# Kernel optimization log

Hardware: AMD Instinct MI355X
Metric: run time of the kernel (lower is better)

Reference implementation:

```python
import jax, jax.numpy as jnp
import numpy as np

EMBED_DIM = 1024
HEAD_DIM = 64
B, S = 8, 2048


def setup_inputs() -> dict:
    key = jax.random.key(0)
    ks = jax.random.split(key, 8)
    s_in = 1.0 / np.sqrt(EMBED_DIM)
    return {
        "x": jax.random.normal(ks[0], (B, S, EMBED_DIM), dtype=jnp.float32),
        "y": jax.random.normal(ks[1], (B, S, EMBED_DIM), dtype=jnp.float32),
        "Wq": jax.random.normal(ks[2], (EMBED_DIM, HEAD_DIM), dtype=jnp.float32) * s_in,
        "bq": jnp.zeros((HEAD_DIM,), dtype=jnp.float32),
        "Wk": jax.random.normal(ks[3], (EMBED_DIM, HEAD_DIM), dtype=jnp.float32) * s_in,
        "bk": jnp.zeros((HEAD_DIM,), dtype=jnp.float32),
        "Wv": jax.random.normal(ks[4], (EMBED_DIM, HEAD_DIM), dtype=jnp.float32) * s_in,
        "bv": jnp.zeros((HEAD_DIM,), dtype=jnp.float32),
    }


def reference(x, y, Wq, bq, Wk, bk, Wv, bv):
    # single-head attention; mask=True -> tril applied PRE-softmax (zeros, not -inf)
    q = jnp.einsum("bse,eh->bsh", y, Wq) + bq  # [B,S,H]
    k = jnp.einsum("bse,eh->bsh", x, Wk) + bk
    v = jnp.einsum("bse,eh->bsh", x, Wv) + bv
    scale = 1.0 / jnp.sqrt(jnp.float32(HEAD_DIM))
    scores = jnp.einsum("bqh,bkh->bqk", q, k) * scale  # [B,S,S]
    scores = jnp.tril(scores)  # faithful: zero upper triangle BEFORE softmax
    attn = jax.nn.softmax(scores, axis=-1)
    return jnp.einsum("bqk,bkh->bqh", attn, v)  # [B,S,H]
```

## Files before the change

### kernel.cpp

```cpp
#include <hip/hip_runtime.h>

#define SEQ 2048
#define EMB 1024
#define HD 64

typedef _Float16 f16x8 __attribute__((ext_vector_type(8)));
typedef _Float16 f16x4 __attribute__((ext_vector_type(4)));
typedef float f32x4 __attribute__((ext_vector_type(4)));

__device__ __forceinline__ f32x4 mfma32(f16x8 a, f16x8 b, f32x4 c) {
    return __builtin_amdgcn_mfma_f32_16x16x32_f16(a, b, c, 0, 0, 0);
}
__device__ __forceinline__ f32x4 mfma16(f16x4 a, f16x4 b, f32x4 c) {
    return __builtin_amdgcn_mfma_f32_16x16x16f16(a, b, c, 0, 0, 0);
}

__global__ __launch_bounds__(256) void wcvt_kernel(
    const float* __restrict__ Wq, const float* __restrict__ Wk,
    const float* __restrict__ Wv, _Float16* __restrict__ Wf)
{
    const int m = blockIdx.x >> 2, nt = blockIdx.x & 3, kq = blockIdx.y;
    const float* __restrict__ W = (m == 0) ? Wq : (m == 1) ? Wk : Wv;
    const int tid = threadIdx.x;
    #pragma unroll
    for (int i = 0; i < 2; ++i) {
        int linear = i * 256 + tid;
        int kc = kq * 8 + (linear >> 6), ln = linear & 63;
        int q8 = (ln >> 4) * 8, l = ln & 15;
        f16x8 w;
        #pragma unroll
        for (int j = 0; j < 8; ++j)
            w[j] = (_Float16)W[(size_t)(kc * 32 + q8 + j) * 64 + nt * 16 + l];
        *(f16x8*)&Wf[((size_t)((m * 4 + nt) * 32 + kc)) * 512 + (size_t)ln * 8] = w;
    }
}

__global__ __launch_bounds__(512, 2) void proj_kernel(
    const float* __restrict__ x, const float* __restrict__ y,
    const _Float16* __restrict__ Wf,
    const float* __restrict__ bq, const float* __restrict__ bk,
    const float* __restrict__ bv,
    _Float16* __restrict__ Qb, _Float16* __restrict__ Kf,
    _Float16* __restrict__ Vf, float* __restrict__ Vts)
{
    const int mode = blockIdx.y;
    const int r0 = blockIdx.x * 128;
    const int tid = threadIdx.x;
    const int wave = tid >> 6, lane = tid & 63;
    const int l15 = lane & 15, quad = lane >> 4;

    __shared__ float TL[128][65];

    const float* __restrict__ src = mode ? x : y;
    const _Float16* __restrict__ WA = Wf + (mode ? 65536 : 0);
    const _Float16* __restrict__ WB = Wf + 131072;

    f32x4 zero = {0.f, 0.f, 0.f, 0.f};
    f32x4 acc0[4], acc1[4];
    #pragma unroll
    for (int i = 0; i < 4; ++i) { acc0[i] = zero; acc1[i] = zero; }

    const float* arow = src + (size_t)(r0 + wave * 16 + l15) * 1024 + quad * 8;
    const int lo8 = lane * 8;

    float4 Aa0, Aa1, Ab0, Ab1;
    f16x8 BqA[4], BqB[4], BvA[4], BvB[4];

    auto LDA = [&](float4& x0, float4& x1, int ch) {
        const float4* p = (const float4*)(arow + ch * 32);
        x0 = p[0]; x1 = p[1];
    };
    auto LDBq = [&](f16x8* d, int ch) {
        #pragma unroll
        for (int nt = 0; nt < 4; ++nt)
            d[nt] = *(const f16x8*)&WA[((size_t)(nt * 32 + ch)) * 512 + lo8];
    };
    auto LDBv = [&](f16x8* d, int ch) {
        #pragma unroll
        for (int nt = 0; nt < 4; ++nt)
            d[nt] = *(const f16x8*)&WB[((size_t)(nt * 32 + ch)) * 512 + lo8];
    };
    auto CVT = [&](float4 a0, float4 a1) {
        f16x8 af;
        af[0] = (_Float16)a0.x; af[1] = (_Float16)a0.y;
        af[2] = (_Float16)a0.z; af[3] = (_Float16)a0.w;
        af[4] = (_Float16)a1.x; af[5] = (_Float16)a1.y;
        af[6] = (_Float16)a1.z; af[7] = (_Float16)a1.w;
        return af;
    };

    LDA(Aa0, Aa1, 0); LDBq(BqA, 0); if (mode) LDBv(BvA, 0);
    LDA(Ab0, Ab1, 1); LDBq(BqB, 1); if (mode) LDBv(BvB, 1);

    #pragma unroll 1
    for (int ch = 0; ch < 32; ch += 2) {
        {
            f16x8 af = CVT(Aa0, Aa1);
            #pragma unroll
            for (int nt = 0; nt < 4; ++nt)
                acc0[nt] = mfma32(af, BqA[nt], acc0[nt]);
            if (mode) {
                #pragma unroll
                for (int nt = 0; nt < 4; ++nt)
                    acc1[nt] = mfma32(af, BvA[nt], acc1[nt]);
            }
            const int nx = (ch + 2) & 31;
            LDA(Aa0, Aa1, nx); LDBq(BqA, nx); if (mode) LDBv(BvA, nx);
        }
        {
            f16x8 af = CVT(Ab0, Ab1);
            #pragma unroll
            for (int nt = 0; nt < 4; ++nt)
                acc0[nt] = mfma32(af, BqB[nt], acc0[nt]);
            if (mode) {
                #pragma unroll
                for (int nt = 0; nt < 4; ++nt)
                    acc1[nt] = mfma32(af, BvB[nt], acc1[nt]);
            }
            const int nx = (ch + 3) & 31;
            LDA(Ab0, Ab1, nx); LDBq(BqB, nx); if (mode) LDBv(BvB, nx);
        }
    }

    const int bb = r0 >> 11, s0 = r0 & (SEQ - 1);

    if (mode == 0) {
        #pragma unroll
        for (int nt = 0; nt < 4; ++nt) {
            int h = nt * 16 + l15;
            float bs = bq[h];
            #pragma unroll
            for (int r = 0; r < 4; ++r) {
                int row = r0 + wave * 16 + quad * 4 + r;
                Qb[(size_t)row * 64 + h] = (_Float16)(acc0[nt][r] + bs);
            }
        }
    } else {
        #pragma unroll
        for (int nt = 0; nt < 4; ++nt) {
            float bs = bk[nt * 16 + l15];
            #pragma unroll
            for (int r = 0; r < 4; ++r)
                TL[wave * 16 + quad * 4 + r][nt * 16 + l15] = acc0[nt][r] + bs;
        }
        __syncthreads();
        {
            int c = tid >> 6, ln = tid & 63;
            const int q8 = (ln >> 4) << 3, l = ln & 15;
            #pragma unroll
            for (int half = 0; half < 2; ++half) {
                f16x8 w;
                #pragma unroll
                for (int j = 0; j < 8; ++j)
                    w[j] = (_Float16)TL[c * 16 + l][half * 32 + q8 + j];
                *(f16x8*)&Kf[(((size_t)(bb * 128 + (s0 >> 4) + c)) * 2 + half) * 512 + ln * 8] = w;
            }
        }
        __syncthreads();
        #pragma unroll
        for (int nt = 0; nt < 4; ++nt) {
            float bs = bv[nt * 16 + l15];
            #pragma unroll
            for (int r = 0; r < 4; ++r)
                TL[wave * 16 + quad * 4 + r][nt * 16 + l15] = acc1[nt][r] + bs;
        }
        __syncthreads();
        {
            int c2 = tid >> 7, hth = (tid >> 6) & 1, ln = tid & 63;
            #pragma unroll
            for (int p = 0; p < 2; ++p) {
                int ht = hth * 2 + p;
                f16x8 w;
                #pragma unroll
                for (int j = 0; j < 8; ++j)
                    w[j] = (_Float16)TL[c2 * 32 + ((j >> 2) << 4) + ((ln >> 4) << 2) + (j & 3)][ht * 16 + (ln & 15)];
                *(f16x8*)&Vf[(((size_t)(bb * 64 + (s0 >> 5) + c2)) * 4 + ht) * 512 + ln * 8] = w;
            }
            int wv = tid >> 6, h = tid & 63;
            float s = 0.f;
            #pragma unroll
            for (int i = 0; i < 16; ++i) s += TL[wv * 16 + i][h];
            Vts[((size_t)bb * 128 + (s0 >> 4) + wv) * 64 + h] = s;
        }
    }
}

__global__ __launch_bounds__(256) void vsuf_kernel(
    const float* __restrict__ Vts, float* __restrict__ Vsuf)
{
    const int b = blockIdx.x, hh = blockIdx.y;
    const int tid = threadIdx.x;
    const int seg = tid >> 5, hl = tid & 31, h = (hh << 5) + hl;
    __shared__ float segsum[8][33];
    float vals[16];
    const float* src = Vts + ((size_t)b * 128 + seg * 16) * 64 + h;
    float s = 0.f;
    #pragma unroll
    for (int i = 0; i < 16; ++i) { vals[i] = src[i * 64]; s += vals[i]; }
    segsum[seg][hl] = s;
    __syncthreads();
    float run = 0.f;
    #pragma unroll
    for (int ss = 7; ss >= 0; --ss) if (ss > seg) run += segsum[ss][hl];
    float* dst = Vsuf + ((size_t)b * 128 + seg * 16) * 64 + h;
    #pragma unroll
    for (int i = 15; i >= 0; --i) { run += vals[i]; dst[i * 64] = run; }
}

__global__ __launch_bounds__(256, 2) void attn_kernel(
    const _Float16* __restrict__ Qb, const _Float16* __restrict__ Kf,
    const _Float16* __restrict__ Vf, const float* __restrict__ Vsuf,
    float* __restrict__ out)
{
    const int b = blockIdx.y;
    const int tp = blockIdx.x;
    const int tid = threadIdx.x;
    const int wave = tid >> 6, lane = tid & 63;
    const int l15 = lane & 15, quad = lane >> 4;

    __shared__ float part[4][32][68];
    __shared__ float lpart[4][32];

    const f16x4 ONES4 = {(_Float16)1.f, (_Float16)1.f, (_Float16)1.f, (_Float16)1.f};
    f32x4 zero = {0.f, 0.f, 0.f, 0.f};

    const _Float16* __restrict__ kfb = Kf + (size_t)b * 131072 + lane * 8;
    const _Float16* __restrict__ vfb = Vf + (size_t)b * 131072 + lane * 8;

    #pragma unroll 1
    for (int sel = 0; sel < 2; ++sel) {
        const int tq = sel ? (63 - tp) : tp;
        const int qbase = tq << 5;
        const int qgA = qbase + l15, qgB = qgA + 16;

        __syncthreads();

        const _Float16* qpA = Qb + ((size_t)(b * SEQ + qbase + l15) << 6);
        const _Float16* qpB = qpA + (16 << 6);
        f16x8 qfA0 = *(const f16x8*)(qpA + quad * 8);
        f16x8 qfA1 = *(const f16x8*)(qpA + 32 + quad * 8);
        f16x8 qfB0 = *(const f16x8*)(qpB + quad * 8);
        f16x8 qfB1 = *(const f16x8*)(qpB + 32 + quad * 8);

        f32x4 accOA[4], accOB[4], accLA = zero, accLB = zero;
        #pragma unroll
        for (int i = 0; i < 4; ++i) { accOA[i] = zero; accOB[i] = zero; }

        f16x8 k0[4], v0[4], k1[4], v1[4];

        auto LDK = [&](f16x8* kd, f16x8* vd, int kc2) {
            const _Float16* kp = kfb + (size_t)kc2 * 2048;
            kd[0] = *(const f16x8*)(kp);
            kd[1] = *(const f16x8*)(kp + 512);
            kd[2] = *(const f16x8*)(kp + 1024);
            kd[3] = *(const f16x8*)(kp + 1536);
            const _Float16* vp = vfb + (size_t)kc2 * 2048;
            vd[0] = *(const f16x8*)(vp);
            vd[1] = *(const f16x8*)(vp + 512);
            vd[2] = *(const f16x8*)(vp + 1024);
            vd[3] = *(const f16x8*)(vp + 1536);
        };

        auto CMP = [&](const f16x8* kd, const f16x8* vd, int kc2) {
            #pragma unroll
            for (int c = 0; c < 2; ++c) {
                f32x4 sA = zero, sB = zero;
                sA = mfma32(kd[2 * c], qfA0, sA);
                sA = mfma32(kd[2 * c + 1], qfA1, sA);
                sB = mfma32(kd[2 * c], qfB0, sB);
                sB = mfma32(kd[2 * c + 1], qfB1, sB);
                const int kqb = (kc2 << 5) + (c << 4) + (quad << 2);
                f16x4 pfA, pfB;
                #pragma unroll
                for (int r = 0; r < 4; ++r) {
                    pfA[r] = (_Float16)((kqb + r <= qgA) ? __expf(sA[r] * 0.125f) : 1.0f);
                    pfB[r] = (_Float16)((kqb + r <= qgB) ? __expf(sB[r] * 0.125f) : 1.0f);
                }
                #pragma unroll
                for (int ht = 0; ht < 4; ++ht) {
                    f16x8 vv = vd[ht];
                    f16x4 vh;
                    if (c == 0) { vh[0] = vv[0]; vh[1] = vv[1]; vh[2] = vv[2]; vh[3] = vv[3]; }
                    else        { vh[0] = vv[4]; vh[1] = vv[5]; vh[2] = vv[6]; vh[3] = vv[7]; }
                    accOA[ht] = mfma16(vh, pfA, accOA[ht]);
                    accOB[ht] = mfma16(vh, pfB, accOB[ht]);
                }
                accLA = mfma16(ONES4, pfA, accLA);
                accLB = mfma16(ONES4, pfB, accLB);
            }
        };

        const int n2 = tq + 1;
        int i = wave;
        LDK(k0, v0, (i < n2) ? i : 0);
        for (; i < n2; i += 8) {
            const int i1 = i + 4;
            LDK(k1, v1, (i1 < n2) ? i1 : i);
            CMP(k0, v0, i);
            const int i2 = i + 8;
            LDK(k0, v0, (i2 < n2) ? i2 : i);
            if (i1 < n2) CMP(k1, v1, i1);
        }

        #pragma unroll
        for (int ht = 0; ht < 4; ++ht)
            #pragma unroll
            for (int r = 0; r < 4; ++r) {
                part[wave][l15][ht * 16 + quad * 4 + r] = accOA[ht][r];
                part[wave][16 + l15][ht * 16 + quad * 4 + r] = accOB[ht][r];
            }
        if (quad == 0) {
            lpart[wave][l15] = accLA[0];
            lpart[wave][16 + l15] = accLB[0];
        }
        __syncthreads();

        {
            const int q = tid >> 3, hb = (tid & 7) << 3;
            f32x4 o0 = zero, o1 = zero;
            float l = 0.f;
            #pragma unroll
            for (int w = 0; w < 4; ++w) {
                l += lpart[w][q];
                o0 = o0 + *(const f32x4*)&part[w][q][hb];
                o1 = o1 + *(const f32x4*)&part[w][q][hb + 4];
            }
            const int tend = 2 * tq + 2;
            const float nOnes = (float)(SEQ - (tend << 4));
            f32x4 cs0 = zero, cs1 = zero;
            if (tend < 128) {
                const float* cp = &Vsuf[((size_t)(b * 128 + tend) << 6) + hb];
                cs0 = *(const f32x4*)(cp);
                cs1 = *(const f32x4*)(cp + 4);
            }
            const float inv = 1.0f / (l + nOnes);
            f32x4 r0 = (o0 + cs0) * inv;
            f32x4 r1 = (o1 + cs1) * inv;
            float* op = &out[((size_t)(b * SEQ + qbase + q) << 6) + hb];
            *(f32x4*)(op) = r0;
            *(f32x4*)(op + 4) = r1;
        }
    }
}

extern "C" void kernel_launch(void* const* d_in, const int* in_sizes, int n_in,
                              void* d_out, int out_size, void* d_ws, size_t ws_size,
                              hipStream_t stream) {
    const float* x  = (const float*)d_in[0];
    const float* y  = (const float*)d_in[1];
    const float* Wq = (const float*)d_in[2];
    const float* bq = (const float*)d_in[3];
    const float* Wk = (const float*)d_in[4];
    const float* bk = (const float*)d_in[5];
    const float* Wv = (const float*)d_in[6];
    const float* bv = (const float*)d_in[7];
    float* out = (float*)d_out;

    char* ws = (char*)d_ws;
    _Float16* Qb  = (_Float16*)(ws);
    _Float16* Kf  = (_Float16*)(ws + (1u << 21));
    _Float16* Vf  = (_Float16*)(ws + (2u << 21));
    _Float16* Wf  = (_Float16*)(ws + (3u << 21));
    float*    Vts = (float*)(ws + (3u << 21) + (512u << 10));
    float*    Vsf = (float*)(ws + (3u << 21) + (768u << 10));

    wcvt_kernel<<<dim3(12, 4), 256, 0, stream>>>(Wq, Wk, Wv, Wf);
    proj_kernel<<<dim3(128, 2), 512, 0, stream>>>(x, y, Wf, bq, bk, bv, Qb, Kf, Vf, Vts);
    vsuf_kernel<<<dim3(8, 2), 256, 0, stream>>>(Vts, Vsf);
    attn_kernel<<<dim3(32, 8), 256, 0, stream>>>(Qb, Kf, Vf, Vsf, out);
}
```

Baseline: 202.5 us.

## Stage projection inputs via direct global-to-LDS loads and split attention tiles per block

The projection kernel now uses 256-thread blocks over 64 rows. Each chunk of the fp32 activation tile is loaded straight into shared memory with global_load_lds and an XOR swizzle, then read back, converted to fp16 and fed to MFMA, replacing per-lane register prefetching. The attention kernel stops pairing a short and a long query tile in one block and launches 64 blocks per batch, one tile each, ordered longest first. This is meant to raise memory-level parallelism and occupancy, but it adds two barriers per chunk and drops register double-buffering in the projection, and it relies on the hardware scheduler for load balance in attention.

```diff
diff --git a/kernel.cpp b/kernel.cpp
--- a/kernel.cpp
+++ b/kernel.cpp
@@ -13,6 +13,12 @@
 }
 __device__ __forceinline__ f32x4 mfma16(f16x4 a, f16x4 b, f32x4 c) {
     return __builtin_amdgcn_mfma_f32_16x16x16f16(a, b, c, 0, 0, 0);
+}
+
+__device__ __forceinline__ void gload_lds16(const float* g, float* l) {
+    __builtin_amdgcn_global_load_lds(
+        (const __attribute__((address_space(1))) unsigned int*)g,
+        (__attribute__((address_space(3))) unsigned int*)l, 16, 0, 0);
 }
 
 __global__ __launch_bounds__(256) void wcvt_kernel(
@@ -35,7 +41,7 @@
     }
 }
 
-__global__ __launch_bounds__(512, 2) void proj_kernel(
+__global__ __launch_bounds__(256, 2) void proj_kernel(
     const float* __restrict__ x, const float* __restrict__ y,
     const _Float16* __restrict__ Wf,
     const float* __restrict__ bq, const float* __restrict__ bk,
@@ -44,12 +50,12 @@
     _Float16* __restrict__ Vf, float* __restrict__ Vts)
 {
     const int mode = blockIdx.y;
-    const int r0 = blockIdx.x * 128;
+    const int r0 = blockIdx.x * 64;
     const int tid = threadIdx.x;
     const int wave = tid >> 6, lane = tid & 63;
     const int l15 = lane & 15, quad = lane >> 4;
 
-    __shared__ float TL[128][65];
+    __shared__ __align__(16) float As[4352];
 
     const float* __restrict__ src = mode ? x : y;
     const _Float16* __restrict__ WA = Wf + (mode ? 65536 : 0);
@@ -60,69 +66,58 @@
     #pragma unroll
     for (int i = 0; i < 4; ++i) { acc0[i] = zero; acc1[i] = zero; }
 
-    const float* arow = src + (size_t)(r0 + wave * 16 + l15) * 1024 + quad * 8;
+    const int jrow = lane >> 4;
+    const int gl = (lane & 15) >> 1, gh = lane & 1;
     const int lo8 = lane * 8;
 
-    float4 Aa0, Aa1, Ab0, Ab1;
-    f16x8 BqA[4], BqB[4], BvA[4], BvB[4];
-
-    auto LDA = [&](float4& x0, float4& x1, int ch) {
-        const float4* p = (const float4*)(arow + ch * 32);
-        x0 = p[0]; x1 = p[1];
-    };
-    auto LDBq = [&](f16x8* d, int ch) {
-        #pragma unroll
-        for (int nt = 0; nt < 4; ++nt)
-            d[nt] = *(const f16x8*)&WA[((size_t)(nt * 32 + ch)) * 512 + lo8];
-    };
-    auto LDBv = [&](f16x8* d, int ch) {
-        #pragma unroll
-        for (int nt = 0; nt < 4; ++nt)
-            d[nt] = *(const f16x8*)&WB[((size_t)(nt * 32 + ch)) * 512 + lo8];
-    };
-    auto CVT = [&](float4 a0, float4 a1) {
-        f16x8 af;
-        af[0] = (_Float16)a0.x; af[1] = (_Float16)a0.y;
-        af[2] = (_Float16)a0.z; af[3] = (_Float16)a0.w;
-        af[4] = (_Float16)a1.x; af[5] = (_Float16)a1.y;
-        af[6] = (_Float16)a1.z; af[7] = (_Float16)a1.w;
-        return af;
-    };
-
-    LDA(Aa0, Aa1, 0); LDBq(BqA, 0); if (mode) LDBv(BvA, 0);
-    LDA(Ab0, Ab1, 1); LDBq(BqB, 1); if (mode) LDBv(BvB, 1);
-
     #pragma unroll 1
-    for (int ch = 0; ch < 32; ch += 2) {
-        {
-            f16x8 af = CVT(Aa0, Aa1);
+    for (int ch = 0; ch < 16; ++ch) {
+        #pragma unroll
+        for (int j = 0; j < 4; ++j) {
+            const int row = wave * 16 + j * 4 + jrow;
+            const float* gp = src + (size_t)(r0 + row) * 1024 + ch * 64
+                              + ((gl ^ (row & 7)) * 8 + gh * 4);
+            gload_lds16(gp, &As[(wave * 16 + j * 4) * 64]);
+        }
+        f16x8 Bq0[4], Bq1[4], Bv0[4], Bv1[4];
+        const int kc0 = ch * 2, kc1 = ch * 2 + 1;
+        #pragma unroll
+        for (int nt = 0; nt < 4; ++nt) {
+            Bq0[nt] = *(const f16x8*)&WA[((size_t)(nt * 32 + kc0)) * 512 + lo8];
+            Bq1[nt] = *(const f16x8*)&WA[((size_t)(nt * 32 + kc1)) * 512 + lo8];
+        }
+        if (mode) {
+            #pragma unroll
+            for (int nt = 0; nt < 4; ++nt) {
+                Bv0[nt] = *(const f16x8*)&WB[((size_t)(nt * 32 + kc0)) * 512 + lo8];
+                Bv1[nt] = *(const f16x8*)&WB[((size_t)(nt * 32 + kc1)) * 512 + lo8];
+            }
+        }
+        __syncthreads();
+        #pragma unroll
+        for (int s = 0; s < 2; ++s) {
+            const float* ap = &As[(wave * 16 + l15) * 64 + (((s * 4 + quad) ^ (l15 & 7)) * 8)];
+            float4 a0 = *(const float4*)ap;
+            float4 a1 = *(const float4*)(ap + 4);
+            f16x8 af;
+            af[0] = (_Float16)a0.x; af[1] = (_Float16)a0.y;
+            af[2] = (_Float16)a0.z; af[3] = (_Float16)a0.w;
+            af[4] = (_Float16)a1.x; af[5] = (_Float16)a1.y;
+            af[6] = (_Float16)a1.z; af[7] = (_Float16)a1.w;
             #pragma unroll
             for (int nt = 0; nt < 4; ++nt)
-                acc0[nt] = mfma32(af, BqA[nt], acc0[nt]);
+                acc0[nt] = mfma32(af, s ? Bq1[nt] : Bq0[nt], acc0[nt]);
             if (mode) {
                 #pragma unroll
                 for (int nt = 0; nt < 4; ++nt)
-                    acc1[nt] = mfma32(af, BvA[nt], acc1[nt]);
-            }
-            const int nx = (ch + 2) & 31;
-            LDA(Aa0, Aa1, nx); LDBq(BqA, nx); if (mode) LDBv(BvA, nx);
-        }
-        {
-            f16x8 af = CVT(Ab0, Ab1);
-            #pragma unroll
-            for (int nt = 0; nt < 4; ++nt)
-                acc0[nt] = mfma32(af, BqB[nt], acc0[nt]);
-            if (mode) {
-                #pragma unroll
-                for (int nt = 0; nt < 4; ++nt)
-                    acc1[nt] = mfma32(af, BvB[nt], acc1[nt]);
-            }
-            const int nx = (ch + 3) & 31;
-            LDA(Ab0, Ab1, nx); LDBq(BqB, nx); if (mode) LDBv(BvB, nx);
-        }
+                    acc1[nt] = mfma32(af, s ? Bv1[nt] : Bv0[nt], acc1[nt]);
+            }
+        }
+        __syncthreads();
     }
 
     const int bb = r0 >> 11, s0 = r0 & (SEQ - 1);
+    float (*TL)[65] = (float(*)[65])As;
 
     if (mode == 0) {
         #pragma unroll
@@ -213,7 +208,7 @@
     float* __restrict__ out)
 {
     const int b = blockIdx.y;
-    const int tp = blockIdx.x;
+    const int tq = 63 - blockIdx.x;
     const int tid = threadIdx.x;
     const int wave = tid >> 6, lane = tid & 63;
     const int l15 = lane & 15, quad = lane >> 4;
@@ -227,119 +222,113 @@
     const _Float16* __restrict__ kfb = Kf + (size_t)b * 131072 + lane * 8;
     const _Float16* __restrict__ vfb = Vf + (size_t)b * 131072 + lane * 8;
 
-    #pragma unroll 1
-    for (int sel = 0; sel < 2; ++sel) {
-        const int tq = sel ? (63 - tp) : tp;
-        const int qbase = tq << 5;
-        const int qgA = qbase + l15, qgB = qgA + 16;
-
-        __syncthreads();
-
-        const _Float16* qpA = Qb + ((size_t)(b * SEQ + qbase + l15) << 6);
-        const _Float16* qpB = qpA + (16 << 6);
-        f16x8 qfA0 = *(const f16x8*)(qpA + quad * 8);
-        f16x8 qfA1 = *(const f16x8*)(qpA + 32 + quad * 8);
-        f16x8 qfB0 = *(const f16x8*)(qpB + quad * 8);
-        f16x8 qfB1 = *(const f16x8*)(qpB + 32 + quad * 8);
-
-        f32x4 accOA[4], accOB[4], accLA = zero, accLB = zero;
-        #pragma unroll
-        for (int i = 0; i < 4; ++i) { accOA[i] = zero; accOB[i] = zero; }
-
-        f16x8 k0[4], v0[4], k1[4], v1[4];
-
-        auto LDK = [&](f16x8* kd, f16x8* vd, int kc2) {
-            const _Float16* kp = kfb + (size_t)kc2 * 2048;
-            kd[0] = *(const f16x8*)(kp);
-            kd[1] = *(const f16x8*)(kp + 512);
-            kd[2] = *(const f16x8*)(kp + 1024);
-            kd[3] = *(const f16x8*)(kp + 1536);
-            const _Float16* vp = vfb + (size_t)kc2 * 2048;
-            vd[0] = *(const f16x8*)(vp);
-            vd[1] = *(const f16x8*)(vp + 512);
-            vd[2] = *(const f16x8*)(vp + 1024);
-            vd[3] = *(const f16x8*)(vp + 1536);
-        };
-
-        auto CMP = [&](const f16x8* kd, const f16x8* vd, int kc2) {
-            #pragma unroll
-            for (int c = 0; c < 2; ++c) {
-                f32x4 sA = zero, sB = zero;
-                sA = mfma32(kd[2 * c], qfA0, sA);
-                sA = mfma32(kd[2 * c + 1], qfA1, sA);
-                sB = mfma32(kd[2 * c], qfB0, sB);
-                sB = mfma32(kd[2 * c + 1], qfB1, sB);
-                const int kqb = (kc2 << 5) + (c << 4) + (quad << 2);
-                f16x4 pfA, pfB;
-                #pragma unroll
-                for (int r = 0; r < 4; ++r) {
-                    pfA[r] = (_Float16)((kqb + r <= qgA) ? __expf(sA[r] * 0.125f) : 1.0f);
-                    pfB[r] = (_Float16)((kqb + r <= qgB) ? __expf(sB[r] * 0.125f) : 1.0f);
-                }
-                #pragma unroll
-                for (int ht = 0; ht < 4; ++ht) {
-                    f16x8 vv = vd[ht];
-                    f16x4 vh;
-                    if (c == 0) { vh[0] = vv[0]; vh[1] = vv[1]; vh[2] = vv[2]; vh[3] = vv[3]; }
-                    else        { vh[0] = vv[4]; vh[1] = vv[5]; vh[2] = vv[6]; vh[3] = vv[7]; }
-                    accOA[ht] = mfma16(vh, pfA, accOA[ht]);
-                    accOB[ht] = mfma16(vh, pfB, accOB[ht]);
-                }
-                accLA = mfma16(ONES4, pfA, accLA);
-                accLB = mfma16(ONES4, pfB, accLB);
-            }
-        };
-
-        const int n2 = tq + 1;
-        int i = wave;
-        LDK(k0, v0, (i < n2) ? i : 0);
-        for (; i < n2; i += 8) {
-            const int i1 = i + 4;
-            LDK(k1, v1, (i1 < n2) ? i1 : i);
-            CMP(k0, v0, i);
-            const int i2 = i + 8;
-            LDK(k0, v0, (i2 < n2) ? i2 : i);
-            if (i1 < n2) CMP(k1, v1, i1);
-        }
-
-        #pragma unroll
-        for (int ht = 0; ht < 4; ++ht)
+    const int qbase = tq << 5;
+    const int qgA = qbase + l15, qgB = qgA + 16;
+
+    const _Float16* qpA = Qb + ((size_t)(b * SEQ + qbase + l15) << 6);
+    const _Float16* qpB = qpA + (16 << 6);
+    f16x8 qfA0 = *(const f16x8*)(qpA + quad * 8);
+    f16x8 qfA1 = *(const f16x8*)(qpA + 32 + quad * 8);
+    f16x8 qfB0 = *(const f16x8*)(qpB + quad * 8);
+    f16x8 qfB1 = *(const f16x8*)(qpB + 32 + quad * 8);
+
+    f32x4 accOA[4], accOB[4], accLA = zero, accLB = zero;
+    #pragma unroll
+    for (int i = 0; i < 4; ++i) { accOA[i] = zero; accOB[i] = zero; }
+
+    f16x8 k0[4], v0[4], k1[4], v1[4];
+
+    auto LDK = [&](f16x8* kd, f16x8* vd, int kc2) {
+        const _Float16* kp = kfb + (size_t)kc2 * 2048;
+        kd[0] = *(const f16x8*)(kp);
+        kd[1] = *(const f16x8*)(kp + 512);
+        kd[2] = *(const f16x8*)(kp + 1024);
+        kd[3] = *(const f16x8*)(kp + 1536);
+        const _Float16* vp = vfb + (size_t)kc2 * 2048;
+        vd[0] = *(const f16x8*)(vp);
+        vd[1] = *(const f16x8*)(vp + 512);
+        vd[2] = *(const f16x8*)(vp + 1024);
+        vd[3] = *(const f16x8*)(vp + 1536);
+    };
+
+    auto CMP = [&](const f16x8* kd, const f16x8* vd, int kc2) {
+        #pragma unroll
+        for (int c = 0; c < 2; ++c) {
+            f32x4 sA = zero, sB = zero;
+            sA = mfma32(kd[2 * c], qfA0, sA);
+            sA = mfma32(kd[2 * c + 1], qfA1, sA);
+            sB = mfma32(kd[2 * c], qfB0, sB);
+            sB = mfma32(kd[2 * c + 1], qfB1, sB);
+            const int kqb = (kc2 << 5) + (c << 4) + (quad << 2);
+            f16x4 pfA, pfB;
             #pragma unroll
             for (int r = 0; r < 4; ++r) {
-                part[wave][l15][ht * 16 + quad * 4 + r] = accOA[ht][r];
-                part[wave][16 + l15][ht * 16 + quad * 4 + r] = accOB[ht][r];
-            }
-        if (quad == 0) {
-            lpart[wave][l15] = accLA[0];
-            lpart[wave][16 + l15] = accLB[0];
-        }
-        __syncthreads();
-
-        {
-            const int q = tid >> 3, hb = (tid & 7) << 3;
-            f32x4 o0 = zero, o1 = zero;
-            float l = 0.f;
-            #pragma unroll
-            for (int w = 0; w < 4; ++w) {
-                l += lpart[w][q];
-                o0 = o0 + *(const f32x4*)&part[w][q][hb];
-                o1 = o1 + *(const f32x4*)&part[w][q][hb + 4];
-            }
-            const int tend = 2 * tq + 2;
-            const float nOnes = (float)(SEQ - (tend << 4));
-            f32x4 cs0 = zero, cs1 = zero;
-            if (tend < 128) {
-                const float* cp = &Vsuf[((size_t)(b * 128 + tend) << 6) + hb];
-                cs0 = *(const f32x4*)(cp);
-                cs1 = *(const f32x4*)(cp + 4);
-            }
-            const float inv = 1.0f / (l + nOnes);
-            f32x4 r0 = (o0 + cs0) * inv;
-            f32x4 r1 = (o1 + cs1) * inv;
-            float* op = &out[((size_t)(b * SEQ + qbase + q) << 6) + hb];
-            *(f32x4*)(op) = r0;
-            *(f32x4*)(op + 4) = r1;
-        }
+                pfA[r] = (_Float16)((kqb + r <= qgA) ? __expf(sA[r] * 0.125f) : 1.0f);
+                pfB[r] = (_Float16)((kqb + r <= qgB) ? __expf(sB[r] * 0.125f) : 1.0f);
+            }
+            #pragma unroll
+            for (int ht = 0; ht < 4; ++ht) {
+                f16x8 vv = vd[ht];
+                f16x4 vh;
+                if (c == 0) { vh[0] = vv[0]; vh[1] = vv[1]; vh[2] = vv[2]; vh[3] = vv[3]; }
+                else        { vh[0] = vv[4]; vh[1] = vv[5]; vh[2] = vv[6]; vh[3] = vv[7]; }
+                accOA[ht] = mfma16(vh, pfA, accOA[ht]);
+                accOB[ht] = mfma16(vh, pfB, accOB[ht]);
+            }
+            accLA = mfma16(ONES4, pfA, accLA);
+            accLB = mfma16(ONES4, pfB, accLB);
+        }
+    };
+
+    const int n2 = tq + 1;
+    int i = wave;
+    LDK(k0, v0, (i < n2) ? i : 0);
+    for (; i < n2; i += 8) {
+        const int i1 = i + 4;
+        LDK(k1, v1, (i1 < n2) ? i1 : i);
+        CMP(k0, v0, i);
+        const int i2 = i + 8;
+        LDK(k0, v0, (i2 < n2) ? i2 : i);
+        if (i1 < n2) CMP(k1, v1, i1);
+    }
+
+    #pragma unroll
+    for (int ht = 0; ht < 4; ++ht)
+        #pragma unroll
+        for (int r = 0; r < 4; ++r) {
+            part[wave][l15][ht * 16 + quad * 4 + r] = accOA[ht][r];
+            part[wave][16 + l15][ht * 16 + quad * 4 + r] = accOB[ht][r];
+        }
+    if (quad == 0) {
+        lpart[wave][l15] = accLA[0];
+        lpart[wave][16 + l15] = accLB[0];
+    }
+    __syncthreads();
+
+    {
+        const int q = tid >> 3, hb = (tid & 7) << 3;
+        f32x4 o0 = zero, o1 = zero;
+        float l = 0.f;
+        #pragma unroll
+        for (int w = 0; w < 4; ++w) {
+            l += lpart[w][q];
+            o0 = o0 + *(const f32x4*)&part[w][q][hb];
+            o1 = o1 + *(const f32x4*)&part[w][q][hb + 4];
+        }
+        const int tend = 2 * tq + 2;
+        const float nOnes = (float)(SEQ - (tend << 4));
+        f32x4 cs0 = zero, cs1 = zero;
+        if (tend < 128) {
+            const float* cp = &Vsuf[((size_t)(b * 128 + tend) << 6) + hb];
+            cs0 = *(const f32x4*)(cp);
+            cs1 = *(const f32x4*)(cp + 4);
+        }
+        const float inv = 1.0f / (l + nOnes);
+        f32x4 r0 = (o0 + cs0) * inv;
+        f32x4 r1 = (o1 + cs1) * inv;
+        float* op = &out[((size_t)(b * SEQ + qbase + q) << 6) + hb];
+        *(f32x4*)(op) = r0;
+        *(f32x4*)(op + 4) = r1;
     }
 }
 
@@ -365,7 +354,7 @@
     float*    Vsf = (float*)(ws + (3u << 21) + (768u << 10));
 
     wcvt_kernel<<<dim3(12, 4), 256, 0, stream>>>(Wq, Wk, Wv, Wf);
-    proj_kernel<<<dim3(128, 2), 512, 0, stream>>>(x, y, Wf, bq, bk, bv, Qb, Kf, Vf, Vts);
+    proj_kernel<<<dim3(256, 2), 256, 0, stream>>>(x, y, Wf, bq, bk, bv, Qb, Kf, Vf, Vts);
     vsuf_kernel<<<dim3(8, 2), 256, 0, stream>>>(Vts, Vsf);
-    attn_kernel<<<dim3(32, 8), 256, 0, stream>>>(Qb, Kf, Vf, Vsf, out);
-}
+    attn_kernel<<<dim3(64, 8), 256, 0, stream>>>(Qb, Kf, Vf, Vsf, out);
+}
```

After: 187.3 us. -7.5%, faster.
